# Kernel tuning notes

Measured on AMD Instinct MI355X. Metric: run time of the kernel, lower is better.

Reference implementation:

```python
import jax, jax.numpy as jnp
import numpy as np

B, S, D = 2, 2048, 2048
H, KV, HD = 32, 8, 64
REP = H // KV  # 4


def setup_inputs() -> dict:
    key = jax.random.key(0)
    ks = jax.random.split(key, 5)
    x = jax.random.normal(ks[0], (B, S, D), jnp.float32)
    # Llama rope frequencies: theta=10000, pairs of adjacent dims
    inv_freq = 1.0 / (10000.0 ** (np.arange(0, HD, 2, dtype=np.float64) / HD))  # [HD/2]
    ang = np.outer(np.arange(S, dtype=np.float64), inv_freq)  # [S, HD/2]
    freqs_cis = jnp.asarray(np.stack([np.cos(ang), np.sin(ang)], axis=-1), jnp.float32)  # [S, HD/2, 2]
    wq = jax.random.normal(ks[1], (H * HD, D), jnp.float32) * 0.02
    wk = jax.random.normal(ks[2], (KV * HD, D), jnp.float32) * 0.02
    wv = jax.random.normal(ks[3], (KV * HD, D), jnp.float32) * 0.02
    wo = jax.random.normal(ks[4], (D, H * HD), jnp.float32) * 0.02
    return {"x": x, "freqs_cis": freqs_cis, "wq": wq, "wk": wk, "wv": wv, "wo": wo}


def _apply_rope(t, cos, sin):
    # t: [B,S,nh,HD]; cos/sin: [S,HD/2]; complex multiply on adjacent pairs
    b, s, nh, hd = t.shape
    t2 = t.reshape(b, s, nh, hd // 2, 2)
    tr, ti = t2[..., 0], t2[..., 1]
    c = cos[None, :, None, :]
    sn = sin[None, :, None, :]
    out = jnp.stack([tr * c - ti * sn, tr * sn + ti * c], axis=-1)
    return out.reshape(b, s, nh, hd)


def reference(x, freqs_cis, wq, wk, wv, wo):
    # QKV projections (torch Linear: y = x @ W.T)
    q = jnp.einsum('bsd,ed->bse', x, wq).reshape(B, S, H, HD)
    k = jnp.einsum('bsd,ed->bse', x, wk).reshape(B, S, KV, HD)
    v = jnp.einsum('bsd,ed->bse', x, wv).reshape(B, S, KV, HD)
    cos, sin = freqs_cis[..., 0], freqs_cis[..., 1]
    q = _apply_rope(q, cos, sin)
    k = _apply_rope(k, cos, sin)
    # GQA without materializing repeated K/V: group query heads by KV head
    qg = q.reshape(B, S, KV, REP, HD)
    scale = 1.0 / jnp.sqrt(jnp.asarray(HD, q.dtype))
    scores = jnp.einsum('bsgrd,btgd->bgrst', qg, k) * scale  # [B,KV,REP,S,S]
    causal = jnp.tril(jnp.ones((S, S), bool))
    scores = jnp.where(causal, scores, -jnp.inf)
    p = jax.nn.softmax(scores, axis=-1)
    o = jnp.einsum('bgrst,btgd->bsgrd', p, v).reshape(B, S, H * HD)
    return jnp.einsum('bse,de->bsd', o, wo)
```

## Files before the change

kernel.cpp:

```cpp
#include <hip/hip_runtime.h>
#include <cstdint>
#include <cstddef>

#define B_ 2
#define S_ 2048
#define D_ 2048
#define H_ 32
#define KV_ 8
#define HD_ 64
#define M_ (B_*S_)
#define EQ_ (H_*HD_)
#define EK_ (KV_*HD_)

typedef unsigned short u16;
typedef __attribute__((ext_vector_type(8))) short s16x8;
typedef __attribute__((ext_vector_type(4))) float f32x4;

#define QSCALE 0.18033688011112042f
#define EXPOFF 15.869645449778564f

#if __has_builtin(__builtin_amdgcn_exp2f)
#define EXP2(x) __builtin_amdgcn_exp2f(x)
#else
#define EXP2(x) __expf((x) * 0.6931471805599453f)
#endif

__device__ __forceinline__ u16 f2bf(float f) {
  unsigned u = __float_as_uint(f);
  u += 0x7fffu + ((u >> 16) & 1u);
  return (u16)(u >> 16);
}
__device__ __forceinline__ unsigned pk2(float a, float b) {
  unsigned ua = __float_as_uint(a) + 0x8000u;
  unsigned ub = __float_as_uint(b) + 0x8000u;
  return __builtin_amdgcn_perm(ub, ua, 0x07060302);
}
__device__ __forceinline__ f32x4 mfma16(s16x8 a, s16x8 b, f32x4 c) {
  return __builtin_amdgcn_mfma_f32_16x16x32_bf16(a, b, c, 0, 0, 0);
}
__device__ __forceinline__ void gl_lds16(const void* g, void* l) {
  __builtin_amdgcn_global_load_lds(
      (const __attribute__((address_space(1))) void*)g,
      (__attribute__((address_space(3))) void*)l, 16, 0, 0);
}

__global__ void cast_all(const float4* __restrict__ x, const float4* __restrict__ wq,
                         const float4* __restrict__ wk, const float4* __restrict__ wv,
                         const float4* __restrict__ wo, ushort4* __restrict__ dst) {
  int i = blockIdx.x * 256 + threadIdx.x;
  const float4* src; int off;
  if (i < 2097152)      { src = x;  off = i; }
  else if (i < 3145728) { src = wq; off = i - 2097152; }
  else if (i < 3407872) { src = wk; off = i - 3145728; }
  else if (i < 3670016) { src = wv; off = i - 3407872; }
  else                  { src = wo; off = i - 3670016; }
  float4 v = src[off];
  ushort4 r;
  r.x = f2bf(v.x); r.y = f2bf(v.y); r.z = f2bf(v.z); r.w = f2bf(v.w);
  dst[i] = r;
}

__global__ __launch_bounds__(256)
void gemm_qkv(const u16* __restrict__ A, const u16* __restrict__ Bw,
              u16* __restrict__ qb, u16* __restrict__ kb, u16* __restrict__ vtb,
              const float* __restrict__ fc) {
  __shared__ __align__(16) u16 As[128 * 64];
  __shared__ __align__(16) u16 Bs[96 * 64];
  const int tid  = threadIdx.x;
  const int lane = tid & 63;
  const int wave = tid >> 6;
  const int m0 = blockIdx.y * 128;
  const int n0 = blockIdx.x * 96;
  const int wm = (wave >> 1) * 64;
  const int wn = (wave & 1) * 48;
  const int l15 = lane & 15;
  const int quad = lane >> 4;

  f32x4 acc[4][3] = {};

  for (int k0 = 0; k0 < D_; k0 += 64) {
    #pragma unroll
    for (int rr = 0; rr < 4; ++rr) {
      int c = tid + rr * 256;
      int row = c >> 3;
      int ksrc = ((c & 7) ^ (row & 7)) * 8;
      gl_lds16(A + (size_t)(m0 + row) * D_ + k0 + ksrc, &As[c * 8]);
    }
    #pragma unroll
    for (int rr = 0; rr < 3; ++rr) {
      int c = tid + rr * 256;
      int row = c >> 3;
      int ksrc = ((c & 7) ^ (row & 7)) * 8;
      gl_lds16(Bw + (size_t)(n0 + row) * D_ + k0 + ksrc, &Bs[c * 8]);
    }
    __syncthreads();

    #pragma unroll
    for (int kc = 0; kc < 2; ++kc) {
      s16x8 af[4], bfr[3];
      #pragma unroll
      for (int mi = 0; mi < 4; ++mi) {
        int row = wm + mi * 16 + l15;
        af[mi]  = *(const s16x8*)&As[row * 64 + (((kc * 4 + quad) ^ (row & 7)) * 8)];
      }
      #pragma unroll
      for (int ni = 0; ni < 3; ++ni) {
        int row = wn + ni * 16 + l15;
        bfr[ni] = *(const s16x8*)&Bs[row * 64 + (((kc * 4 + quad) ^ (row & 7)) * 8)];
      }
      #pragma unroll
      for (int mi = 0; mi < 4; ++mi)
        #pragma unroll
        for (int ni = 0; ni < 3; ++ni)
          acc[mi][ni] = mfma16(af[mi], bfr[ni], acc[mi][ni]);
    }
    __syncthreads();
  }

  const float sg = (l15 & 1) ? 1.f : -1.f;
  #pragma unroll
  for (int mi = 0; mi < 4; ++mi) {
    #pragma unroll
    for (int ni = 0; ni < 3; ++ni) {
      const int col = n0 + wn + ni * 16 + l15;
      if (col < 2560) {
        const bool isQ = (col < 2048);
        u16* dst = isQ ? qb : kb;
        const int ncol0 = isQ ? 0 : 2048;
        const int ndim  = isQ ? EQ_ : EK_;
        const float scale = isQ ? QSCALE : 1.0f;
        const int ip = (col & 63) >> 1;
        #pragma unroll
        for (int r = 0; r < 4; ++r) {
          int row = m0 + wm + mi * 16 + quad * 4 + r;
          const float* fr = fc + (size_t)(row & (S_ - 1)) * 64;
          float c  = fr[ip * 2];
          float sn = fr[ip * 2 + 1];
          float v = acc[mi][ni][r];
          float p = __shfl_xor(v, 1, 64);
          float o = (v * c + sg * (p * sn)) * scale;
          dst[(size_t)row * ndim + col - ncol0] = f2bf(o);
        }
      } else {
        const int vcol = col - 2560;
        uint2 w;
        w.x = pk2(acc[mi][ni][0], acc[mi][ni][1]);
        w.y = pk2(acc[mi][ni][2], acc[mi][ni][3]);
        *(uint2*)(vtb + (size_t)vcol * M_ + m0 + wm + mi * 16 + quad * 4) = w;
      }
    }
  }
}

__global__ __launch_bounds__(256)
void gemm_o(const u16* __restrict__ A, const u16* __restrict__ Bw, float* __restrict__ C,
            int Ndim, int Kdim) {
  __shared__ __align__(16) u16 As[64 * 64];
  __shared__ __align__(16) u16 Bs[128 * 64];
  const int tid  = threadIdx.x;
  const int lane = tid & 63;
  const int wave = tid >> 6;
  const int m0 = blockIdx.y * 64;
  const int n0 = blockIdx.x * 128;
  const int wm = (wave >> 1) * 32;
  const int wn = (wave & 1) * 64;
  const int l15 = lane & 15;
  const int quad = lane >> 4;

  f32x4 acc[2][4] = {};

  for (int k0 = 0; k0 < Kdim; k0 += 64) {
    #pragma unroll
    for (int rr = 0; rr < 2; ++rr) {
      int c = tid + rr * 256;
      int row = c >> 3;
      int ksrc = ((c & 7) ^ (row & 7)) * 8;
      gl_lds16(A + (size_t)(m0 + row) * Kdim + k0 + ksrc, &As[c * 8]);
    }
    #pragma unroll
    for (int rr = 0; rr < 4; ++rr) {
      int c = tid + rr * 256;
      int row = c >> 3;
      int ksrc = ((c & 7) ^ (row & 7)) * 8;
      gl_lds16(Bw + (size_t)(n0 + row) * Kdim + k0 + ksrc, &Bs[c * 8]);
    }
    __syncthreads();

    #pragma unroll
    for (int kc = 0; kc < 2; ++kc) {
      s16x8 af[2], bfr[4];
      #pragma unroll
      for (int mi = 0; mi < 2; ++mi) {
        int row = wm + mi * 16 + l15;
        af[mi]  = *(const s16x8*)&As[row * 64 + (((kc * 4 + quad) ^ (row & 7)) * 8)];
      }
      #pragma unroll
      for (int ni = 0; ni < 4; ++ni) {
        int row = wn + ni * 16 + l15;
        bfr[ni] = *(const s16x8*)&Bs[row * 64 + (((kc * 4 + quad) ^ (row & 7)) * 8)];
      }
      #pragma unroll
      for (int mi = 0; mi < 2; ++mi)
        #pragma unroll
        for (int ni = 0; ni < 4; ++ni)
          acc[mi][ni] = mfma16(af[mi], bfr[ni], acc[mi][ni]);
    }
    __syncthreads();
  }

  #pragma unroll
  for (int mi = 0; mi < 2; ++mi) {
    #pragma unroll
    for (int r = 0; r < 4; ++r) {
      int row = m0 + wm + mi * 16 + quad * 4 + r;
      size_t base = (size_t)row * Ndim + n0 + wn;
      #pragma unroll
      for (int ni = 0; ni < 4; ++ni)
        C[base + ni * 16 + l15] = acc[mi][ni][r];
    }
  }
}

__global__ __launch_bounds__(256, 4)
void flash_attn(const u16* __restrict__ qb, const u16* __restrict__ kb,
                const u16* __restrict__ vtb, u16* __restrict__ ob) {
  const int bx = blockIdx.x;
  const int h  = blockIdx.y;
  const int b  = blockIdx.z;
  const int g  = h >> 2;
  const int tid  = threadIdx.x;
  const int lane = tid & 63;
  const int wave = tid >> 6;
  const int l15  = lane & 15;
  const int quad = lane >> 4;
  const int kq   = quad * 8;

  const int Tlo = bx, Thi = 31 - bx;
  const int n_lo = Tlo + 1, n_hi = Thi + 1;
  const int rL = Tlo * 64 + wave * 16;
  const int rH = Thi * 64 + wave * 16;
  const int rowL = rL + l15;
  const int rowH = rH + l15;

  __shared__ __align__(16) u16 Ks[2][8 * 512];
  __shared__ __align__(16) u16 Vs[2][8 * 512];
  __shared__ __align__(16) u16 Pl[4][2][16 * 72];

  u16* PbL = &Pl[wave][0][0];
  u16* PbH = &Pl[wave][1][0];

  const u16* qpL = qb + (size_t)(b * S_ + rL + l15) * EQ_ + h * HD_;
  const u16* qpH = qb + (size_t)(b * S_ + rH + l15) * EQ_ + h * HD_;
  s16x8 qL0 = *(const s16x8*)(qpL + kq);
  s16x8 qL1 = *(const s16x8*)(qpL + 32 + kq);
  s16x8 qH0 = *(const s16x8*)(qpH + kq);
  s16x8 qH1 = *(const s16x8*)(qpH + 32 + kq);

  f32x4 OL[4] = {}, OH[4] = {};
  float sumL = 0.f, sumH = 0.f;

  const int sw = wave & 1;
  const bool doK = (wave < 2);

  const u16* stbase;
  size_t     tstride;
  int        ldoff;
  if (doK) {
    stbase  = kb + (size_t)(b * S_ + lane) * EK_ + g * HD_ + sw * 32;
    tstride = (size_t)64 * EK_;
  } else {
    stbase  = vtb + (size_t)(g * HD_ + lane) * M_ + b * S_ + sw * 32;
    tstride = 64;
  }
  ldoff = sw * 4 * 512 + lane * 8;
  u16* lbuf0 = doK ? &Ks[0][0] : &Vs[0][0];
  u16* lbuf1 = doK ? &Ks[1][0] : &Vs[1][0];

  #pragma unroll
  for (int r = 0; r < 4; ++r)
    gl_lds16(stbase + r * 8, lbuf0 + ldoff + r * 512);
  __syncthreads();

  for (int kt = 0; kt < n_hi; ++kt) {
    const int t0 = kt * 64;
    const u16* kcur = &Ks[kt & 1][0];
    const u16* vcur = &Vs[kt & 1][0];

    if (kt + 1 < n_hi) {
      u16* dst = (((kt + 1) & 1) ? lbuf1 : lbuf0) + ldoff;
      const u16* src = stbase + (size_t)(kt + 1) * tstride;
      #pragma unroll
      for (int r = 0; r < 4; ++r)
        gl_lds16(src + r * 8, dst + r * 512);
    }

    const bool do_lo = (kt < n_lo);
    const bool mH = (kt == n_hi - 1);
    const bool mL = (kt == n_lo - 1);

    #pragma unroll
    for (int ts = 0; ts < 4; ++ts) {
      s16x8 k0 = *(const s16x8*)&kcur[quad * 512 + (ts * 16 + l15) * 8];
      s16x8 k1 = *(const s16x8*)&kcur[(4 + quad) * 512 + (ts * 16 + l15) * 8];
      const int tb = t0 + ts * 16 + quad * 4;
      {
        f32x4 s = {};
        s = mfma16(k0, qH0, s);
        s = mfma16(k1, qH1, s);
        if (mH) {
          #pragma unroll
          for (int r = 0; r < 4; ++r) if (tb + r > rowH) s[r] = -1e30f;
        }
        float p0 = EXP2(s[0] - EXPOFF), p1 = EXP2(s[1] - EXPOFF);
        float p2 = EXP2(s[2] - EXPOFF), p3 = EXP2(s[3] - EXPOFF);
        sumH += (p0 + p1) + (p2 + p3);
        uint2 w; w.x = pk2(p0, p1); w.y = pk2(p2, p3);
        *(uint2*)&PbH[l15 * 72 + ts * 16 + quad * 4] = w;
      }
      if (do_lo) {
        f32x4 s = {};
        s = mfma16(k0, qL0, s);
        s = mfma16(k1, qL1, s);
        if (mL) {
          #pragma unroll
          for (int r = 0; r < 4; ++r) if (tb + r > rowL) s[r] = -1e30f;
        }
        float p0 = EXP2(s[0] - EXPOFF), p1 = EXP2(s[1] - EXPOFF);
        float p2 = EXP2(s[2] - EXPOFF), p3 = EXP2(s[3] - EXPOFF);
        sumL += (p0 + p1) + (p2 + p3);
        uint2 w; w.x = pk2(p0, p1); w.y = pk2(p2, p3);
        *(uint2*)&PbL[l15 * 72 + ts * 16 + quad * 4] = w;
      }
    }

    s16x8 pH0 = *(const s16x8*)&PbH[l15 * 72 + kq];
    s16x8 pH1 = *(const s16x8*)&PbH[l15 * 72 + 32 + kq];
    s16x8 pL0 = {}, pL1 = {};
    if (do_lo) {
      pL0 = *(const s16x8*)&PbL[l15 * 72 + kq];
      pL1 = *(const s16x8*)&PbL[l15 * 72 + 32 + kq];
    }

    #pragma unroll
    for (int df = 0; df < 4; ++df) {
      s16x8 v0 = *(const s16x8*)&vcur[quad * 512 + (df * 16 + l15) * 8];
      s16x8 v1 = *(const s16x8*)&vcur[(4 + quad) * 512 + (df * 16 + l15) * 8];
      OH[df] = mfma16(v1, pH1, mfma16(v0, pH0, OH[df]));
      if (do_lo) OL[df] = mfma16(v1, pL1, mfma16(v0, pL0, OL[df]));
    }

    __syncthreads();
  }

  sumH += __shfl_xor(sumH, 16, 64); sumH += __shfl_xor(sumH, 32, 64);
  sumL += __shfl_xor(sumL, 16, 64); sumL += __shfl_xor(sumL, 32, 64);
  float invH = 1.f / sumH, invL = 1.f / sumL;

  {
    u16* op = ob + (size_t)(b * S_ + rowH) * EQ_ + h * HD_;
    #pragma unroll
    for (int df = 0; df < 4; ++df) {
      uint2 w;
      w.x = pk2(OH[df][0] * invH, OH[df][1] * invH);
      w.y = pk2(OH[df][2] * invH, OH[df][3] * invH);
      *(uint2*)(op + df * 16 + quad * 4) = w;
    }
  }
  {
    u16* op = ob + (size_t)(b * S_ + rowL) * EQ_ + h * HD_;
    #pragma unroll
    for (int df = 0; df < 4; ++df) {
      uint2 w;
      w.x = pk2(OL[df][0] * invL, OL[df][1] * invL);
      w.y = pk2(OL[df][2] * invL, OL[df][3] * invL);
      *(uint2*)(op + df * 16 + quad * 4) = w;
    }
  }
}

extern "C" void kernel_launch(void* const* d_in, const int* in_sizes, int n_in,
                              void* d_out, int out_size, void* d_ws, size_t ws_size,
                              hipStream_t stream) {
  (void)in_sizes; (void)n_in; (void)out_size; (void)ws_size;
  const float* x  = (const float*)d_in[0];
  const float* fc = (const float*)d_in[1];
  const float* wq = (const float*)d_in[2];
  const float* wk = (const float*)d_in[3];
  const float* wv = (const float*)d_in[4];
  const float* wo = (const float*)d_in[5];
  float* out = (float*)d_out;
  char* ws = (char*)d_ws;

  u16* xb  = (u16*)(ws);
  u16* wqb = (u16*)(ws + 16777216);
  u16* wob = (u16*)(ws + 29360128);
  u16* qb  = (u16*)(ws + 37748736);
  u16* kb  = (u16*)(ws + 54525952);
  u16* vtb = (u16*)(ws + 58720256);
  u16* ob  = (u16*)(ws + 62914560);

  cast_all<<<18432, 256, 0, stream>>>((const float4*)x, (const float4*)wq,
                                      (const float4*)wk, (const float4*)wv,
                                      (const float4*)wo, (ushort4*)ws);

  gemm_qkv<<<dim3(32, 32), 256, 0, stream>>>(xb, wqb, qb, kb, vtb, fc);

  flash_attn<<<dim3(16, 32, 2), 256, 0, stream>>>(qb, kb, vtb, ob);

  gemm_o<<<dim3(16, 64), 256, 0, stream>>>(ob, wob, out, D_, EQ_);
}
```

Before: 324.5 us.

## Single-buffer V tile loaded per iteration and swizzle P scratch layout

V is now single-buffered: each iteration the V waves load the current V tile and an extra barrier is placed before the PV MFMAs, while K stays double-buffered with prefetch. The P scratch buffer drops its 72-element padded rows for 64-element rows with an XOR swizzle to avoid LDS bank conflicts. This cuts LDS usage, which may allow higher occupancy, but it adds a second barrier per iteration and exposes V load latency that was previously hidden behind the QK stage.

After: 301.3 us. 1.08x faster.

```diff
diff --git a/kernel.cpp b/kernel.cpp
--- a/kernel.cpp
+++ b/kernel.cpp
@@ -243,11 +243,12 @@
   const int rowH = rH + l15;
 
   __shared__ __align__(16) u16 Ks[2][8 * 512];
-  __shared__ __align__(16) u16 Vs[2][8 * 512];
-  __shared__ __align__(16) u16 Pl[4][2][16 * 72];
-
-  u16* PbL = &Pl[wave][0][0];
-  u16* PbH = &Pl[wave][1][0];
+  __shared__ __align__(16) u16 Vs[8 * 512];
+  __shared__ __align__(16) u16 Pl[4][2][16 * 64];
+
+  char* PbL = (char*)&Pl[wave][0][0];
+  char* PbH = (char*)&Pl[wave][1][0];
+  const int pm = (l15 & 7) << 4;
 
   const u16* qpL = qb + (size_t)(b * S_ + rL + l15) * EQ_ + h * HD_;
   const u16* qpH = qb + (size_t)(b * S_ + rH + l15) * EQ_ + h * HD_;
@@ -264,7 +265,6 @@
 
   const u16* stbase;
   size_t     tstride;
-  int        ldoff;
   if (doK) {
     stbase  = kb + (size_t)(b * S_ + lane) * EK_ + g * HD_ + sw * 32;
     tstride = (size_t)64 * EK_;
@@ -272,26 +272,32 @@
     stbase  = vtb + (size_t)(g * HD_ + lane) * M_ + b * S_ + sw * 32;
     tstride = 64;
   }
-  ldoff = sw * 4 * 512 + lane * 8;
-  u16* lbuf0 = doK ? &Ks[0][0] : &Vs[0][0];
-  u16* lbuf1 = doK ? &Ks[1][0] : &Vs[1][0];
-
-  #pragma unroll
-  for (int r = 0; r < 4; ++r)
-    gl_lds16(stbase + r * 8, lbuf0 + ldoff + r * 512);
+  const int ldoff = sw * 4 * 512 + lane * 8;
+
+  if (doK) {
+    #pragma unroll
+    for (int r = 0; r < 4; ++r)
+      gl_lds16(stbase + r * 8, &Ks[0][ldoff + r * 512]);
+  }
   __syncthreads();
 
   for (int kt = 0; kt < n_hi; ++kt) {
     const int t0 = kt * 64;
     const u16* kcur = &Ks[kt & 1][0];
-    const u16* vcur = &Vs[kt & 1][0];
-
-    if (kt + 1 < n_hi) {
-      u16* dst = (((kt + 1) & 1) ? lbuf1 : lbuf0) + ldoff;
-      const u16* src = stbase + (size_t)(kt + 1) * tstride;
+
+    if (doK) {
+      if (kt + 1 < n_hi) {
+        const u16* src = stbase + (size_t)(kt + 1) * tstride;
+        u16* dst = &Ks[(kt + 1) & 1][ldoff];
+        #pragma unroll
+        for (int r = 0; r < 4; ++r)
+          gl_lds16(src + r * 8, dst + r * 512);
+      }
+    } else {
+      const u16* src = stbase + (size_t)kt * tstride;
       #pragma unroll
       for (int r = 0; r < 4; ++r)
-        gl_lds16(src + r * 8, dst + r * 512);
+        gl_lds16(src + r * 8, &Vs[ldoff + r * 512]);
     }
 
     const bool do_lo = (kt < n_lo);
@@ -315,7 +321,7 @@
         float p2 = EXP2(s[2] - EXPOFF), p3 = EXP2(s[3] - EXPOFF);
         sumH += (p0 + p1) + (p2 + p3);
         uint2 w; w.x = pk2(p0, p1); w.y = pk2(p2, p3);
-        *(uint2*)&PbH[l15 * 72 + ts * 16 + quad * 4] = w;
+        *(uint2*)(PbH + l15 * 128 + ((ts * 32 + quad * 8) ^ pm)) = w;
       }
       if (do_lo) {
         f32x4 s = {};
@@ -329,22 +335,24 @@
         float p2 = EXP2(s[2] - EXPOFF), p3 = EXP2(s[3] - EXPOFF);
         sumL += (p0 + p1) + (p2 + p3);
         uint2 w; w.x = pk2(p0, p1); w.y = pk2(p2, p3);
-        *(uint2*)&PbL[l15 * 72 + ts * 16 + quad * 4] = w;
-      }
-    }
-
-    s16x8 pH0 = *(const s16x8*)&PbH[l15 * 72 + kq];
-    s16x8 pH1 = *(const s16x8*)&PbH[l15 * 72 + 32 + kq];
+        *(uint2*)(PbL + l15 * 128 + ((ts * 32 + quad * 8) ^ pm)) = w;
+      }
+    }
+
+    s16x8 pH0 = *(const s16x8*)(PbH + l15 * 128 + ((quad * 16) ^ pm));
+    s16x8 pH1 = *(const s16x8*)(PbH + l15 * 128 + ((64 + quad * 16) ^ pm));
     s16x8 pL0 = {}, pL1 = {};
     if (do_lo) {
-      pL0 = *(const s16x8*)&PbL[l15 * 72 + kq];
-      pL1 = *(const s16x8*)&PbL[l15 * 72 + 32 + kq];
-    }
+      pL0 = *(const s16x8*)(PbL + l15 * 128 + ((quad * 16) ^ pm));
+      pL1 = *(const s16x8*)(PbL + l15 * 128 + ((64 + quad * 16) ^ pm));
+    }
+
+    __syncthreads();
 
     #pragma unroll
     for (int df = 0; df < 4; ++df) {
-      s16x8 v0 = *(const s16x8*)&vcur[quad * 512 + (df * 16 + l15) * 8];
-      s16x8 v1 = *(const s16x8*)&vcur[(4 + quad) * 512 + (df * 16 + l15) * 8];
+      s16x8 v0 = *(const s16x8*)&Vs[quad * 512 + (df * 16 + l15) * 8];
+      s16x8 v1 = *(const s16x8*)&Vs[(4 + quad) * 512 + (df * 16 + l15) * 8];
       OH[df] = mfma16(v1, pH1, mfma16(v0, pH0, OH[df]));
       if (do_lo) OL[df] = mfma16(v1, pL1, mfma16(v0, pL0, OL[df]));
     }
```
